# Optimization experiments

Hardware: AMD Instinct MI355X
Metric: run time of the kernel (lower is better)

The kernel has to match this reference:

```python
import jax, jax.numpy as jnp
import numpy as np

B, S_SRC, S_TGT, H, V = 32, 128, 64, 300, 32000


def setup_inputs() -> dict:
    key = jax.random.key(0)
    ks = jax.random.split(key, 16)

    def n(k, shape, scale=0.05):
        return jax.random.normal(k, shape, dtype=jnp.float32) * scale

    return {
        "x": jax.random.randint(ks[0], (B, S_SRC), 0, V),
        "y": jax.random.randint(ks[1], (B, S_TGT), 0, V),
        "h0": jax.random.normal(ks[2], (B, H), dtype=jnp.float32),  # encoder initNormState (L=1 squeezed)
        "EN": n(ks[3], (V, H)),
        "ZH": n(ks[4], (V, H)),
        "enc_Wih": n(ks[5], (H, H)),
        "enc_Whh": n(ks[6], (H, H)),
        "enc_bih": n(ks[7], (H,)),
        "enc_bhh": n(ks[8], (H,)),
        "dec_Wih": n(ks[9], (H, H)),
        "dec_Whh": n(ks[10], (H, H)),
        "dec_bih": n(ks[11], (H,)),
        "dec_bhh": n(ks[12], (H,)),
        "W_out": n(ks[13], (V, H)),
        "b_out": n(ks[14], (V,)),
    }


def reference(x, y, h0, EN, ZH, enc_Wih, enc_Whh, enc_bih, enc_bhh,
              dec_Wih, dec_Whh, dec_bih, dec_bhh, W_out, b_out):
    # ---- encoder: 1-layer tanh RNN over source embeddings ----
    xe = EN[x]  # [B, S_src, H]

    def enc_step(h, xt):  # xt: [B, H]
        h = jnp.tanh(xt @ enc_Wih.T + enc_bih + h @ enc_Whh.T + enc_bhh)
        return h, None

    c, _ = jax.lax.scan(enc_step, h0, jnp.swapaxes(xe, 0, 1))  # c: [B, H] final hidden

    # ---- decoder: original loop always feeds encoder state c (never the updated
    # hidden) to the RNNCell; with teacher forcing (start_TF_rate=1.0) every step
    # uses y_in[t], so all T steps vectorize into one batched computation. ----
    ye = ZH[y]  # [B, T, H]
    dec_state_term = c @ dec_Whh.T + dec_bhh  # [B, H], shared across all steps
    h_dec = jnp.tanh(ye @ dec_Wih.T + dec_bih + dec_state_term[:, None, :])  # [B, T, H]
    out = h_dec @ W_out.T + b_out  # [B, T, V]
    return out
```

## Files before the change

### kernel.cpp

```cpp
#include <hip/hip_runtime.h>
#include <hip/hip_bf16.h>
#include <stdint.h>

#define BB 32
#define S_SRC 128
#define S_TGT 64
#define H 300
#define VV 32000
#define M_ROWS (BB * S_TGT)
#define KP 320

typedef __attribute__((ext_vector_type(8))) __bf16 bf16x8;
typedef __attribute__((ext_vector_type(4))) float f32x4;
typedef __attribute__((ext_vector_type(4))) unsigned short u16x4;

__device__ inline unsigned short f2bf(float f) {
    union { float f; unsigned u; } v; v.f = f;
    unsigned r = (v.u + 0x7FFF + ((v.u >> 16) & 1)) >> 16;
    return (unsigned short)r;
}

__device__ __forceinline__ void gl_lds16(const void* g, void* l) {
    __builtin_amdgcn_global_load_lds(
        (const __attribute__((address_space(1))) void*)g,
        (__attribute__((address_space(3))) void*)l, 16, 0, 0);
}

__global__ void transpose4(const float* W0, const float* W1, const float* W2,
                           const float* W3, float* dst) {
    const float* srcs[4] = {W0, W1, W2, W3};
    const float* src = srcs[blockIdx.z];
    float* d = dst + (size_t)blockIdx.z * (H * H);
    __shared__ float tile[32][33];
    int j0 = blockIdx.y * 32, k0 = blockIdx.x * 32;
    for (int r = threadIdx.y; r < 32; r += blockDim.y) {
        int j = j0 + r, k = k0 + threadIdx.x;
        tile[r][threadIdx.x] = (j < H && k < H) ? src[(size_t)j * H + k] : 0.f;
    }
    __syncthreads();
    for (int r = threadIdx.y; r < 32; r += blockDim.y) {
        int k = k0 + r, j = j0 + threadIdx.x;
        if (k < H && j < H) d[(size_t)k * H + j] = tile[threadIdx.x][r];
    }
}

#define RPB 8
__global__ __launch_bounds__(192) void pproj(const int* __restrict__ x,
                                             const float* __restrict__ EN,
                                             const float* __restrict__ WihT,
                                             const float* __restrict__ bih,
                                             const float* __restrict__ bhh,
                                             float* __restrict__ P) {
    __shared__ float xe[RPB][H];
    int m0 = blockIdx.x * RPB;
    int tid = threadIdx.x;
    for (int r = 0; r < RPB; ++r) {
        int idx = x[m0 + r];
        for (int c = tid; c < H; c += 192) xe[r][c] = EN[(size_t)idx * H + c];
    }
    __syncthreads();
    if (tid < 150) {
        int j = tid * 2;
        float a0[RPB], a1[RPB];
#pragma unroll
        for (int r = 0; r < RPB; ++r) { a0[r] = 0.f; a1[r] = 0.f; }
        const float* wp = WihT + j;
        for (int k = 0; k < H; ++k) {
            float2 w = *reinterpret_cast<const float2*>(wp + (size_t)k * H);
#pragma unroll
            for (int r = 0; r < RPB; ++r) {
                float xv = xe[r][k];
                a0[r] += xv * w.x; a1[r] += xv * w.y;
            }
        }
        float b0 = bih[j] + bhh[j], b1 = bih[j + 1] + bhh[j + 1];
#pragma unroll
        for (int r = 0; r < RPB; ++r) {
            P[(size_t)(m0 + r) * H + j]     = a0[r] + b0;
            P[(size_t)(m0 + r) * H + j + 1] = a1[r] + b1;
        }
    }
}

#define ENC_T 512
__global__ __launch_bounds__(ENC_T, 2) void encoder2(const float* __restrict__ h0,
                                                     const float* __restrict__ P,
                                                     const float* __restrict__ Whh,
                                                     float* __restrict__ c) {
    __shared__ float hbuf[304];
    __shared__ float part[3][304];
    int b = blockIdx.x, tid = threadIdx.x;
    int s = tid / 160;
    int jp = tid - s * 160;
    bool act = (s < 3) && (jp < 150);
    int j0 = jp * 2;

    float4 w0[25], w1[25];
    if (act) {
        const float* p0 = Whh + (size_t)j0 * H + s * 100;
        const float* p1 = p0 + H;
#pragma unroll
        for (int i = 0; i < 25; ++i) {
            w0[i] = *reinterpret_cast<const float4*>(p0 + i * 4);
            w1[i] = *reinterpret_cast<const float4*>(p1 + i * 4);
        }
    }
    for (int i = tid; i < H; i += ENC_T) hbuf[i] = h0[(size_t)b * H + i];
    __syncthreads();

    const float* Pb = P + (size_t)b * S_SRC * H;
    for (int t = 0; t < S_SRC; ++t) {
        float2 pv = make_float2(0.f, 0.f);
        if (s == 0 && jp < 150)
            pv = *reinterpret_cast<const float2*>(Pb + (size_t)t * H + j0);
        if (act) {
            float a0 = 0.f, a1 = 0.f;
            const float* hr = hbuf + s * 100;
#pragma unroll
            for (int i = 0; i < 25; ++i) {
                float4 hv = *reinterpret_cast<const float4*>(hr + i * 4);
                a0 += hv.x * w0[i].x; a1 += hv.x * w1[i].x;
                a0 += hv.y * w0[i].y; a1 += hv.y * w1[i].y;
                a0 += hv.z * w0[i].z; a1 += hv.z * w1[i].z;
                a0 += hv.w * w0[i].w; a1 += hv.w * w1[i].w;
            }
            *reinterpret_cast<float2*>(&part[s][j0]) = make_float2(a0, a1);
        }
        __syncthreads();
        if (s == 0 && jp < 150) {
            float s0 = part[0][j0]     + part[1][j0]     + part[2][j0]     + pv.x;
            float s1 = part[0][j0 + 1] + part[1][j0 + 1] + part[2][j0 + 1] + pv.y;
            *reinterpret_cast<float2*>(&hbuf[j0]) = make_float2(tanhf(s0), tanhf(s1));
        }
        __syncthreads();
    }
    for (int i = tid; i < H; i += ENC_T) c[(size_t)b * H + i] = hbuf[i];
}

__global__ __launch_bounds__(192) void sdec(const float* __restrict__ c,
                                            const float* __restrict__ WhhT_d,
                                            const float* __restrict__ bih_d,
                                            const float* __restrict__ bhh_d,
                                            float* __restrict__ s2) {
    __shared__ float cl[H];
    int b = blockIdx.x, tid = threadIdx.x;
    for (int k = tid; k < H; k += 192) cl[k] = c[(size_t)b * H + k];
    __syncthreads();
    if (tid < 150) {
        int j = tid * 2;
        float a0 = 0.f, a1 = 0.f;
        const float* wp = WhhT_d + j;
        for (int k = 0; k < H; ++k) {
            float2 w = *reinterpret_cast<const float2*>(wp + (size_t)k * H);
            a0 += cl[k] * w.x; a1 += cl[k] * w.y;
        }
        s2[(size_t)b * H + j]     = a0 + bih_d[j] + bhh_d[j];
        s2[(size_t)b * H + j + 1] = a1 + bih_d[j + 1] + bhh_d[j + 1];
    }
}

__global__ __launch_bounds__(192) void hdec_k(const int* __restrict__ y,
                                              const float* __restrict__ ZH,
                                              const float* __restrict__ WihT_d,
                                              const float* __restrict__ s2,
                                              unsigned short* __restrict__ hdec) {
    __shared__ float ye[RPB][H];
    int m0 = blockIdx.x * RPB;
    int tid = threadIdx.x;
    for (int r = 0; r < RPB; ++r) {
        int idx = y[m0 + r];
        for (int c = tid; c < H; c += 192) ye[r][c] = ZH[(size_t)idx * H + c];
    }
    __syncthreads();
    if (tid < 150) {
        int j = tid * 2;
        float a0[RPB], a1[RPB];
#pragma unroll
        for (int r = 0; r < RPB; ++r) { a0[r] = 0.f; a1[r] = 0.f; }
        const float* wp = WihT_d + j;
        for (int k = 0; k < H; ++k) {
            float2 w = *reinterpret_cast<const float2*>(wp + (size_t)k * H);
#pragma unroll
            for (int r = 0; r < RPB; ++r) {
                float xv = ye[r][k];
                a0[r] += xv * w.x; a1[r] += xv * w.y;
            }
        }
#pragma unroll
        for (int r = 0; r < RPB; ++r) {
            int m = m0 + r;
            int b = m >> 6;
            float sv0 = s2[(size_t)b * H + j], sv1 = s2[(size_t)b * H + j + 1];
            hdec[(size_t)m * KP + j]     = f2bf(tanhf(a0[r] + sv0));
            hdec[(size_t)m * KP + j + 1] = f2bf(tanhf(a1[r] + sv1));
        }
    } else if (tid < 160) {
        int j = 300 + (tid - 150) * 2;
#pragma unroll
        for (int r = 0; r < RPB; ++r) {
            hdec[(size_t)(m0 + r) * KP + j]     = 0;
            hdec[(size_t)(m0 + r) * KP + j + 1] = 0;
        }
    }
}

__global__ __launch_bounds__(256) void wcvt(const float* __restrict__ W,
                                            unsigned short* __restrict__ Wb) {
    int id = blockIdx.x * 256 + threadIdx.x;
    int row = id / 80, c = id - row * 80;
    int k = c * 4;
    u16x4 o;
    if (k < H) {
        float4 f = *reinterpret_cast<const float4*>(W + (size_t)row * H + k);
        o[0] = f2bf(f.x); o[1] = f2bf(f.y); o[2] = f2bf(f.z); o[3] = f2bf(f.w);
    } else {
        o[0] = 0; o[1] = 0; o[2] = 0; o[3] = 0;
    }
    *reinterpret_cast<u16x4*>(Wb + (size_t)row * KP + k) = o;
}

__global__ __launch_bounds__(256) void gemm2(const unsigned short* __restrict__ A,
                                             const unsigned short* __restrict__ Wb,
                                             const float* __restrict__ bout,
                                             float* __restrict__ out) {
    __shared__ unsigned short Al[2][128 * 64];
    __shared__ unsigned short Blds[2][128 * 64];
    int tid = threadIdx.x;
    int lane = tid & 63, wv = tid >> 6;
    int wm = wv >> 1, wn = wv & 1;

    int orig = blockIdx.x;
    int wg = (orig & 7) * 500 + (orig >> 3);
    int mi = wg & 15, ni = wg >> 4;
    int m0 = mi * 128, n0 = ni * 128;

    int rowb = tid >> 3;
    int sc2 = (tid & 7) ^ (rowb & 7);

    f32x4 acc[4][4];
    f32x4 zero = {0.f, 0.f, 0.f, 0.f};
#pragma unroll
    for (int i = 0; i < 4; ++i)
#pragma unroll
        for (int j = 0; j < 4; ++j) acc[i][j] = zero;

#pragma unroll
    for (int i = 0; i < 4; ++i) {
        int row = i * 32 + rowb;
        gl_lds16(A + (size_t)(m0 + row) * KP + sc2 * 8, &Al[0][(i * 256 + tid) * 8]);
    }
#pragma unroll
    for (int i = 0; i < 4; ++i) {
        int row = i * 32 + rowb;
        gl_lds16(Wb + (size_t)(n0 + row) * KP + sc2 * 8, &Blds[0][(i * 256 + tid) * 8]);
    }

    for (int t = 0; t < 5; ++t) {
        __syncthreads();
        int buf = t & 1;
        bf16x8 af[2][4], bb[2][4];
#pragma unroll
        for (int ks = 0; ks < 2; ++ks)
#pragma unroll
            for (int i = 0; i < 4; ++i) {
                int ch = (ks * 4 + (lane >> 4)) ^ (lane & 7);
                int rowA = wm * 64 + i * 16 + (lane & 15);
                af[ks][i] = *reinterpret_cast<const bf16x8*>(&Al[buf][rowA * 64 + ch * 8]);
                int rowB = wn * 64 + i * 16 + (lane & 15);
                bb[ks][i] = *reinterpret_cast<const bf16x8*>(&Blds[buf][rowB * 64 + ch * 8]);
            }
        if (t < 4) {
            int k0 = (t + 1) * 64, nb = buf ^ 1;
#pragma unroll
            for (int i = 0; i < 4; ++i) {
                int row = i * 32 + rowb;
                gl_lds16(A + (size_t)(m0 + row) * KP + k0 + sc2 * 8,
                         &Al[nb][(i * 256 + tid) * 8]);
            }
#pragma unroll
            for (int i = 0; i < 4; ++i) {
                int row = i * 32 + rowb;
                gl_lds16(Wb + (size_t)(n0 + row) * KP + k0 + sc2 * 8,
                         &Blds[nb][(i * 256 + tid) * 8]);
            }
        }
#pragma unroll
        for (int ks = 0; ks < 2; ++ks)
#pragma unroll
            for (int i = 0; i < 4; ++i)
#pragma unroll
                for (int j = 0; j < 4; ++j)
                    acc[i][j] = __builtin_amdgcn_mfma_f32_16x16x32_bf16(
                        af[ks][i], bb[ks][j], acc[i][j], 0, 0, 0);
    }

#pragma unroll
    for (int j = 0; j < 4; ++j) {
        int col = n0 + wn * 64 + j * 16 + (lane & 15);
        float bo = bout[col];
#pragma unroll
        for (int i = 0; i < 4; ++i) {
            int rb = m0 + wm * 64 + i * 16 + (lane >> 4) * 4;
            f32x4 v = acc[i][j];
#pragma unroll
            for (int r = 0; r < 4; ++r)
                out[(size_t)(rb + r) * VV + col] = v[r] + bo;
        }
    }
}

#define LDSW 40
__global__ __launch_bounds__(256) void gemm_out(const unsigned short* __restrict__ A,
                                                const float* __restrict__ W,
                                                const float* __restrict__ bout,
                                                float* __restrict__ out) {
    __shared__ __align__(16) unsigned short Alds[128 * LDSW];
    __shared__ __align__(16) unsigned short Bl[128 * LDSW];
    int tid = threadIdx.x;
    int lane = tid & 63, wv = tid >> 6;
    int wm = wv >> 1, wn = wv & 1;
    int m0 = blockIdx.y * 128, n0 = blockIdx.x * 128;

    f32x4 acc[4][4];
    f32x4 zero = {0.f, 0.f, 0.f, 0.f};
#pragma unroll
    for (int i = 0; i < 4; ++i)
#pragma unroll
        for (int jj = 0; jj < 4; ++jj) acc[i][jj] = zero;

    for (int k0 = 0; k0 < KP; k0 += 32) {
#pragma unroll
        for (int s = 0; s < 2; ++s) {
            int slot = tid + s * 256;
            int row = slot >> 2, c16 = slot & 3;
            uint4 v = *reinterpret_cast<const uint4*>(
                &A[(size_t)(m0 + row) * KP + k0 + c16 * 8]);
            *reinterpret_cast<uint4*>(&Alds[row * LDSW + c16 * 8]) = v;
        }
#pragma unroll
        for (int s = 0; s < 2; ++s) {
            int slot = tid + s * 256;
            int row = slot >> 2, c8 = slot & 3;
            int k = k0 + c8 * 8;
            __align__(16) unsigned short tmp[8];
            if (k + 7 < H) {
                const float* src = &W[(size_t)(n0 + row) * H + k];
                float4 f0 = *reinterpret_cast<const float4*>(src);
                float4 f1 = *reinterpret_cast<const float4*>(src + 4);
                tmp[0] = f2bf(f0.x); tmp[1] = f2bf(f0.y);
                tmp[2] = f2bf(f0.z); tmp[3] = f2bf(f0.w);
                tmp[4] = f2bf(f1.x); tmp[5] = f2bf(f1.y);
                tmp[6] = f2bf(f1.z); tmp[7] = f2bf(f1.w);
            } else {
#pragma unroll
                for (int jv = 0; jv < 8; ++jv) {
                    int kk = k + jv;
                    tmp[jv] = (kk < H) ? f2bf(W[(size_t)(n0 + row) * H + kk])
                                       : (unsigned short)0;
                }
            }
            *reinterpret_cast<uint4*>(&Bl[row * LDSW + c8 * 8]) =
                *reinterpret_cast<const uint4*>(tmp);
        }
        __syncthreads();
        bf16x8 af[4], bfm[4];
#pragma unroll
        for (int i = 0; i < 4; ++i) {
            int row = wm * 64 + i * 16 + (lane & 15);
            af[i] = *reinterpret_cast<const bf16x8*>(&Alds[row * LDSW + (lane >> 4) * 8]);
        }
#pragma unroll
        for (int i = 0; i < 4; ++i) {
            int row = wn * 64 + i * 16 + (lane & 15);
            bfm[i] = *reinterpret_cast<const bf16x8*>(&Bl[row * LDSW + (lane >> 4) * 8]);
        }
#pragma unroll
        for (int i = 0; i < 4; ++i)
#pragma unroll
            for (int jj = 0; jj < 4; ++jj)
                acc[i][jj] = __builtin_amdgcn_mfma_f32_16x16x32_bf16(
                    af[i], bfm[jj], acc[i][jj], 0, 0, 0);
        __syncthreads();
    }
#pragma unroll
    for (int jj = 0; jj < 4; ++jj) {
        int col = n0 + wn * 64 + jj * 16 + (lane & 15);
        float bo = bout[col];
#pragma unroll
        for (int i = 0; i < 4; ++i) {
            int rb = m0 + wm * 64 + i * 16 + (lane >> 4) * 4;
            f32x4 v = acc[i][jj];
#pragma unroll
            for (int r = 0; r < 4; ++r)
                out[(size_t)(rb + r) * VV + col] = v[r] + bo;
        }
    }
}

extern "C" void kernel_launch(void* const* d_in, const int* in_sizes, int n_in,
                              void* d_out, int out_size, void* d_ws, size_t ws_size,
                              hipStream_t stream) {
    const int*   x       = (const int*)d_in[0];
    const int*   y       = (const int*)d_in[1];
    const float* h0      = (const float*)d_in[2];
    const float* EN      = (const float*)d_in[3];
    const float* ZH      = (const float*)d_in[4];
    const float* enc_Wih = (const float*)d_in[5];
    const float* enc_Whh = (const float*)d_in[6];
    const float* enc_bih = (const float*)d_in[7];
    const float* enc_bhh = (const float*)d_in[8];
    const float* dec_Wih = (const float*)d_in[9];
    const float* dec_Whh = (const float*)d_in[10];
    const float* dec_bih = (const float*)d_in[11];
    const float* dec_bhh = (const float*)d_in[12];
    const float* W_out   = (const float*)d_in[13];
    const float* b_out   = (const float*)d_in[14];
    float* out = (float*)d_out;
    char* base = (char*)d_ws;

    const size_t needA = 23307520, needB = 7742720;
    bool bigws = (ws_size >= needA);
    if (!bigws && ws_size < needB) return;

    float* WT = (float*)base;
    float* P  = (float*)(base + 1440000);
    float *c_, *s2_;
    unsigned short *hdec, *Wb = nullptr;
    if (bigws) {
        Wb   = (unsigned short*)(base + 1440000);
        c_   = (float*)(base + 21920000);
        s2_  = (float*)(base + 21958400);
        hdec = (unsigned short*)(base + 21996800);
    } else {
        c_   = (float*)(base + 6355200);
        s2_  = (float*)(base + 6393600);
        hdec = (unsigned short*)(base + 6432000);
    }

    transpose4<<<dim3(10, 10, 4), dim3(32, 8), 0, stream>>>(
        enc_Wih, enc_Whh, dec_Wih, dec_Whh, WT);
    pproj<<<(BB * S_SRC) / RPB, 192, 0, stream>>>(x, EN, WT, enc_bih, enc_bhh, P);
    encoder2<<<BB, ENC_T, 0, stream>>>(h0, P, enc_Whh, c_);
    sdec<<<BB, 192, 0, stream>>>(c_, WT + 270000, dec_bih, dec_bhh, s2_);
    hdec_k<<<M_ROWS / RPB, 192, 0, stream>>>(y, ZH, WT + 180000, s2_, hdec);
    if (bigws) {
        wcvt<<<(VV * 80) / 256, 256, 0, stream>>>(W_out, Wb);
        gemm2<<<4000, 256, 0, stream>>>(hdec, Wb, b_out, out);
    } else {
        gemm_out<<<dim3(VV / 128, M_ROWS / 128), 256, 0, stream>>>(hdec, W_out, b_out, out);
    }
}
```

Baseline: 318.4 us.

## Use fp16 dot2 in encoder recurrence, fast tanh, and earlier GEMM prefetch

The encoder recurrence now stores weights and hidden state as packed fp16 and uses fdot2 instructions, halving register and LDS footprint per step. The tanh-plus-sum reduction is spread across 150 threads instead of 150 in one slice. Library tanhf is replaced by an exp2/rcp approximation in the encoder and decoder. The output GEMM issues next-tile loads before reading fragments from LDS. The fp16 hidden state and approximate tanh lower accuracy over 128 recurrent steps.

```diff
diff --git a/kernel.cpp b/kernel.cpp
--- a/kernel.cpp
+++ b/kernel.cpp
@@ -13,11 +13,31 @@
 typedef __attribute__((ext_vector_type(8))) __bf16 bf16x8;
 typedef __attribute__((ext_vector_type(4))) float f32x4;
 typedef __attribute__((ext_vector_type(4))) unsigned short u16x4;
+typedef __attribute__((ext_vector_type(2))) __fp16 f16x2;
+
+#if defined(__has_builtin)
+#if __has_builtin(__builtin_amdgcn_fdot2)
+#define HAVE_FDOT2 1
+#endif
+#endif
 
 __device__ inline unsigned short f2bf(float f) {
     union { float f; unsigned u; } v; v.f = f;
     unsigned r = (v.u + 0x7FFF + ((v.u >> 16) & 1)) >> 16;
     return (unsigned short)r;
+}
+
+__device__ __forceinline__ float ftanh(float x) {
+    float e = __builtin_amdgcn_exp2f(x * 2.8853900817779268f);
+    return 1.0f - 2.0f * __builtin_amdgcn_rcpf(e + 1.0f);
+}
+
+__device__ __forceinline__ float fdot2(f16x2 a, f16x2 b, float c) {
+#ifdef HAVE_FDOT2
+    return __builtin_amdgcn_fdot2(a, b, c, false);
+#else
+    return c + (float)a.x * (float)b.x + (float)a.y * (float)b.y;
+#endif
 }
 
 __device__ __forceinline__ void gl_lds16(const void* g, void* l) {
@@ -83,58 +103,76 @@
 }
 
 #define ENC_T 512
-__global__ __launch_bounds__(ENC_T, 2) void encoder2(const float* __restrict__ h0,
+__global__ __launch_bounds__(ENC_T, 2) void encoder3(const float* __restrict__ h0,
                                                      const float* __restrict__ P,
                                                      const float* __restrict__ Whh,
                                                      float* __restrict__ c) {
-    __shared__ float hbuf[304];
-    __shared__ float part[3][304];
+    __shared__ __align__(16) f16x2 hbuf2[160];
+    __shared__ __align__(16) float part[3][304];
     int b = blockIdx.x, tid = threadIdx.x;
     int s = tid / 160;
     int jp = tid - s * 160;
     bool act = (s < 3) && (jp < 150);
     int j0 = jp * 2;
-
-    float4 w0[25], w1[25];
+    int jq = s * 50 + jp;
+    bool red = (s < 3) && (jp < 50);
+
+    f16x2 w0[50], w1[50];
     if (act) {
         const float* p0 = Whh + (size_t)j0 * H + s * 100;
         const float* p1 = p0 + H;
 #pragma unroll
         for (int i = 0; i < 25; ++i) {
-            w0[i] = *reinterpret_cast<const float4*>(p0 + i * 4);
-            w1[i] = *reinterpret_cast<const float4*>(p1 + i * 4);
-        }
-    }
-    for (int i = tid; i < H; i += ENC_T) hbuf[i] = h0[(size_t)b * H + i];
+            float4 f0 = *reinterpret_cast<const float4*>(p0 + i * 4);
+            float4 f1 = *reinterpret_cast<const float4*>(p1 + i * 4);
+            w0[2 * i]     = __builtin_amdgcn_cvt_pkrtz(f0.x, f0.y);
+            w0[2 * i + 1] = __builtin_amdgcn_cvt_pkrtz(f0.z, f0.w);
+            w1[2 * i]     = __builtin_amdgcn_cvt_pkrtz(f1.x, f1.y);
+            w1[2 * i + 1] = __builtin_amdgcn_cvt_pkrtz(f1.z, f1.w);
+        }
+    }
+    if (red) {
+        float2 hv = *reinterpret_cast<const float2*>(h0 + (size_t)b * H + 2 * jq);
+        hbuf2[jq] = __builtin_amdgcn_cvt_pkrtz(hv.x, hv.y);
+    }
     __syncthreads();
 
     const float* Pb = P + (size_t)b * S_SRC * H;
     for (int t = 0; t < S_SRC; ++t) {
         float2 pv = make_float2(0.f, 0.f);
-        if (s == 0 && jp < 150)
-            pv = *reinterpret_cast<const float2*>(Pb + (size_t)t * H + j0);
+        if (red)
+            pv = *reinterpret_cast<const float2*>(Pb + (size_t)t * H + 2 * jq);
         if (act) {
             float a0 = 0.f, a1 = 0.f;
-            const float* hr = hbuf + s * 100;
+            const uint2* hp = reinterpret_cast<const uint2*>(hbuf2 + s * 50);
 #pragma unroll
             for (int i = 0; i < 25; ++i) {
-                float4 hv = *reinterpret_cast<const float4*>(hr + i * 4);
-                a0 += hv.x * w0[i].x; a1 += hv.x * w1[i].x;
-                a0 += hv.y * w0[i].y; a1 += hv.y * w1[i].y;
-                a0 += hv.z * w0[i].z; a1 += hv.z * w1[i].z;
-                a0 += hv.w * w0[i].w; a1 += hv.w * w1[i].w;
+                uint2 u = hp[i];
+                f16x2 h0v = __builtin_bit_cast(f16x2, u.x);
+                f16x2 h1v = __builtin_bit_cast(f16x2, u.y);
+                a0 = fdot2(w0[2 * i], h0v, a0);
+                a0 = fdot2(w0[2 * i + 1], h1v, a0);
+                a1 = fdot2(w1[2 * i], h0v, a1);
+                a1 = fdot2(w1[2 * i + 1], h1v, a1);
             }
             *reinterpret_cast<float2*>(&part[s][j0]) = make_float2(a0, a1);
         }
         __syncthreads();
-        if (s == 0 && jp < 150) {
-            float s0 = part[0][j0]     + part[1][j0]     + part[2][j0]     + pv.x;
-            float s1 = part[0][j0 + 1] + part[1][j0 + 1] + part[2][j0 + 1] + pv.y;
-            *reinterpret_cast<float2*>(&hbuf[j0]) = make_float2(tanhf(s0), tanhf(s1));
+        if (red) {
+            float2 q0 = *reinterpret_cast<const float2*>(&part[0][2 * jq]);
+            float2 q1 = *reinterpret_cast<const float2*>(&part[1][2 * jq]);
+            float2 q2 = *reinterpret_cast<const float2*>(&part[2][2 * jq]);
+            float s0 = q0.x + q1.x + q2.x + pv.x;
+            float s1 = q0.y + q1.y + q2.y + pv.y;
+            hbuf2[jq] = __builtin_amdgcn_cvt_pkrtz(ftanh(s0), ftanh(s1));
         }
         __syncthreads();
     }
-    for (int i = tid; i < H; i += ENC_T) c[(size_t)b * H + i] = hbuf[i];
+    if (red) {
+        f16x2 hv = hbuf2[jq];
+        *reinterpret_cast<float2*>(c + (size_t)b * H + 2 * jq) =
+            make_float2((float)hv.x, (float)hv.y);
+    }
 }
 
 __global__ __launch_bounds__(192) void sdec(const float* __restrict__ c,
@@ -191,8 +229,8 @@
             int m = m0 + r;
             int b = m >> 6;
             float sv0 = s2[(size_t)b * H + j], sv1 = s2[(size_t)b * H + j + 1];
-            hdec[(size_t)m * KP + j]     = f2bf(tanhf(a0[r] + sv0));
-            hdec[(size_t)m * KP + j + 1] = f2bf(tanhf(a1[r] + sv1));
+            hdec[(size_t)m * KP + j]     = f2bf(ftanh(a0[r] + sv0));
+            hdec[(size_t)m * KP + j + 1] = f2bf(ftanh(a1[r] + sv1));
         }
     } else if (tid < 160) {
         int j = 300 + (tid - 150) * 2;
@@ -258,6 +296,21 @@
     for (int t = 0; t < 5; ++t) {
         __syncthreads();
         int buf = t & 1;
+        if (t < 4) {
+            int k0 = (t + 1) * 64, nb = buf ^ 1;
+#pragma unroll
+            for (int i = 0; i < 4; ++i) {
+                int row = i * 32 + rowb;
+                gl_lds16(A + (size_t)(m0 + row) * KP + k0 + sc2 * 8,
+                         &Al[nb][(i * 256 + tid) * 8]);
+            }
+#pragma unroll
+            for (int i = 0; i < 4; ++i) {
+                int row = i * 32 + rowb;
+                gl_lds16(Wb + (size_t)(n0 + row) * KP + k0 + sc2 * 8,
+                         &Blds[nb][(i * 256 + tid) * 8]);
+            }
+        }
         bf16x8 af[2][4], bb[2][4];
 #pragma unroll
         for (int ks = 0; ks < 2; ++ks)
@@ -269,21 +322,6 @@
                 int rowB = wn * 64 + i * 16 + (lane & 15);
                 bb[ks][i] = *reinterpret_cast<const bf16x8*>(&Blds[buf][rowB * 64 + ch * 8]);
             }
-        if (t < 4) {
-            int k0 = (t + 1) * 64, nb = buf ^ 1;
-#pragma unroll
-            for (int i = 0; i < 4; ++i) {
-                int row = i * 32 + rowb;
-                gl_lds16(A + (size_t)(m0 + row) * KP + k0 + sc2 * 8,
-                         &Al[nb][(i * 256 + tid) * 8]);
-            }
-#pragma unroll
-            for (int i = 0; i < 4; ++i) {
-                int row = i * 32 + rowb;
-                gl_lds16(Wb + (size_t)(n0 + row) * KP + k0 + sc2 * 8,
-                         &Blds[nb][(i * 256 + tid) * 8]);
-            }
-        }
 #pragma unroll
         for (int ks = 0; ks < 2; ++ks)
 #pragma unroll
@@ -440,7 +478,7 @@
     transpose4<<<dim3(10, 10, 4), dim3(32, 8), 0, stream>>>(
         enc_Wih, enc_Whh, dec_Wih, dec_Whh, WT);
     pproj<<<(BB * S_SRC) / RPB, 192, 0, stream>>>(x, EN, WT, enc_bih, enc_bhh, P);
-    encoder2<<<BB, ENC_T, 0, stream>>>(h0, P, enc_Whh, c_);
+    encoder3<<<BB, ENC_T, 0, stream>>>(h0, P, enc_Whh, c_);
     sdec<<<BB, 192, 0, stream>>>(c_, WT + 270000, dec_bih, dec_bhh, s2_);
     hdec_k<<<M_ROWS / RPB, 192, 0, stream>>>(y, ZH, WT + 180000, s2_, hdec);
     if (bigws) {
```

New measurement: 279.8 us. -12.1%, faster.
